# Kernel tuning notes

Hardware: AMD Instinct MI355X
Metric: run time of the kernel (lower is better)

The kernel has to match this reference:

```python
import jax, jax.numpy as jnp
import numpy as np

NUM_HEADS = 32
NUM_FEATURES = 512
CPH = NUM_FEATURES // NUM_HEADS  # 16


def _grouped_1x1(x_flat, w, b, groups):
    # x_flat: (B, Cin); w: (Cout, Cin//groups); b: (Cout,)
    B, Cin = x_flat.shape
    Cout = w.shape[0]
    xg = x_flat.reshape(B, groups, Cin // groups)
    wg = w.reshape(groups, Cout // groups, Cin // groups)
    out = jnp.einsum('bgi,goi->bgo', xg, wg).reshape(B, Cout) + b
    return out


def _attend(x, w, b):
    # x: (B, C, H, W, Z) zero-mean input; w: (num_heads, CPH); b: (num_heads,)
    B, C, H, W, Z = x.shape
    N = H * W * Z
    xr = x.reshape(B, NUM_HEADS, CPH, N)
    # grouped 1x1 conv producing one attention logit map per head
    logits = jnp.einsum('bhcn,hc->bhn', xr, w) + b[None, :, None]
    attn = jax.nn.softmax(logits, axis=-1)  # softmax over spatial
    res = jnp.einsum('bhcn,bhn->bhc', xr, attn)  # weighted pooling
    return res.reshape(B, C, 1, 1, 1)


def setup_inputs() -> dict:
    key = jax.random.key(0)
    ks = jax.random.split(key, 7)
    C = NUM_FEATURES
    x = jax.random.normal(ks[0], (4, C, 32, 32, 32), dtype=jnp.float32)
    # P module: conv1 C->C/2 groups=32, conv2 C/2->C groups=32 (kaiming-like scale)
    pw1 = jax.random.normal(ks[1], (C // 2, C // NUM_HEADS), dtype=jnp.float32) * np.float32(np.sqrt(2.0 / (C // 2)))
    pb1 = jnp.zeros((C // 2,), dtype=jnp.float32)
    pw2 = jax.random.normal(ks[2], (C, (C // 2) // NUM_HEADS), dtype=jnp.float32) * np.float32(np.sqrt(2.0 / C))
    pb2 = jnp.zeros((C,), dtype=jnp.float32)
    kw = jax.random.normal(ks[3], (NUM_HEADS, CPH), dtype=jnp.float32) * np.float32(np.sqrt(2.0 / NUM_HEADS))
    kb = jnp.zeros((NUM_HEADS,), dtype=jnp.float32)
    qw = jax.random.normal(ks[4], (NUM_HEADS, CPH), dtype=jnp.float32) * np.float32(np.sqrt(2.0 / NUM_HEADS))
    qb = jnp.zeros((NUM_HEADS,), dtype=jnp.float32)
    return {"x": x, "pw1": pw1, "pb1": pb1, "pw2": pw2, "pb2": pb2,
            "kw": kw, "kb": kb, "qw": qw, "qb": qb}


def reference(x, pw1, pb1, pw2, pb2, kw, kb, qw, qb):
    B, C, H, W, Z = x.shape
    mu = x.mean(axis=(2, 3, 4), keepdims=True)  # (B,C,1,1,1)
    x_mu = x - mu
    # P: grouped bottleneck MLP on mu with sigmoid gate
    h1 = jax.nn.relu(_grouped_1x1(mu.reshape(B, C), pw1, pb1, NUM_HEADS))
    P = jax.nn.sigmoid(_grouped_1x1(h1, pw2, pb2, NUM_HEADS)).reshape(B, C, 1, 1, 1)
    K = _attend(x_mu, kw, kb)
    Q = _attend(x_mu, qw, qb)
    y = (x + K - Q) * P
    dp = jnp.mean(K * Q, axis=1, keepdims=True)  # (B,1,1,1,1)
    return (y, dp)
```

## Files before the change

### kernel.cpp

```cpp
#include <hip/hip_runtime.h>
#include <math.h>

namespace {

constexpr int B = 4;
constexpr int C = 512;
constexpr int NH = 32;
constexpr int CPH = 16;
constexpr int N = 32 * 32 * 32;
constexpr int NPW = 128;
constexpr long YSIZE = (long)B * C * N;

typedef float f4v __attribute__((ext_vector_type(4)));

__device__ inline float wrs(float v) {
#pragma unroll
  for (int o = 32; o > 0; o >>= 1) v += __shfl_xor(v, o);
  return v;
}

template <int CTRL>
__device__ __forceinline__ float dppAdd(float v) {
  const int r = __builtin_amdgcn_update_dpp(
      0, __float_as_int(v), CTRL, 0xF, 0xF, true);
  return v + __int_as_float(r);
}
__device__ __forceinline__ float waveSum(float v) {
  v = dppAdd<0xB1>(v);
  v = dppAdd<0x4E>(v);
  v = dppAdd<0x124>(v);
  v = dppAdd<0x128>(v);
  v += __shfl_xor(v, 16);
  v += __shfl_xor(v, 32);
  return v;
}

__global__ __launch_bounds__(256, 4) void kA(const float* __restrict__ x,
                                             const float* __restrict__ kw,
                                             const float* __restrict__ qw,
                                             float* __restrict__ prec) {
  const int b = blockIdx.z, h = blockIdx.y, j = blockIdx.x;
  const int t = threadIdx.x, lane = t & 63, wid = t >> 6;
  const float* xs = x + ((long)(b * C + h * CPH)) * N + (long)j * 1024 + t * 4;

  float4 xv[CPH];
#pragma unroll
  for (int c = 0; c < CPH; ++c) xv[c] = *(const float4*)(xs + (long)c * N);

  float4 lk = make_float4(0.f, 0.f, 0.f, 0.f);
  float4 lq = make_float4(0.f, 0.f, 0.f, 0.f);
#pragma unroll
  for (int c = 0; c < CPH; ++c) {
    const float wkc = kw[h * CPH + c], wqc = qw[h * CPH + c];
    lk.x += xv[c].x * wkc; lk.y += xv[c].y * wkc;
    lk.z += xv[c].z * wkc; lk.w += xv[c].w * wkc;
    lq.x += xv[c].x * wqc; lq.y += xv[c].y * wqc;
    lq.z += xv[c].z * wqc; lq.w += xv[c].w * wqc;
  }
  const float4 ek = make_float4(__expf(lk.x), __expf(lk.y),
                                __expf(lk.z), __expf(lk.w));
  const float4 eq = make_float4(__expf(lq.x), __expf(lq.y),
                                __expf(lq.z), __expf(lq.w));
  float sK = waveSum((ek.x + ek.y) + (ek.z + ek.w));
  float sQ = waveSum((eq.x + eq.y) + (eq.z + eq.w));

  float outv = 0.f;
#pragma unroll
  for (int c = 0; c < CPH; ++c) {
    float dk = (xv[c].x * ek.x + xv[c].y * ek.y) + (xv[c].z * ek.z + xv[c].w * ek.w);
    float dq = (xv[c].x * eq.x + xv[c].y * eq.y) + (xv[c].z * eq.z + xv[c].w * eq.w);
    float cs = (xv[c].x + xv[c].y) + (xv[c].z + xv[c].w);
    dk = waveSum(dk);
    dq = waveSum(dq);
    cs = waveSum(cs);
    if (lane == c)      outv = dk;
    if (lane == c + 16) outv = dq;
    if (lane == c + 32) outv = cs;
  }
  if (lane == 48) outv = sK;
  if (lane == 49) outv = sQ;

  const long pj = ((long)(b * NH + h)) * NPW + j * 4 + wid;
  prec[pj * 64 + lane] = outv;
}

__global__ __launch_bounds__(512) void k4(const float* __restrict__ prec,
                                          const float* __restrict__ pw1,
                                          const float* __restrict__ pb1,
                                          const float* __restrict__ pw2,
                                          const float* __restrict__ pb2,
                                          float* __restrict__ scale,
                                          float* __restrict__ offset,
                                          float* __restrict__ dpOut) {
  const int b = blockIdx.x;
  const int c = threadIdx.x;
  const int h = c >> 4, i = c & 15;
  const float* rec = prec + ((long)(b * NH + h)) * NPW * 64;

  float dk = 0.f, dq = 0.f, cs = 0.f, sk = 0.f, sq = 0.f;
  for (int j = 0; j < NPW; ++j) {
    dk += rec[j * 64 + i];
    dq += rec[j * 64 + 16 + i];
    cs += rec[j * 64 + 32 + i];
    sk += rec[j * 64 + 48];
    sq += rec[j * 64 + 49];
  }
  const float mu = cs * (1.f / N);
  const float Kv = dk / sk - mu;
  const float Qv = dq / sq - mu;

  __shared__ float muS[C], h1S[256];
  muS[c] = mu;
  __syncthreads();
  if (c < 256) {
    const int g = c >> 3;
    float a = pb1[c];
#pragma unroll
    for (int k = 0; k < 16; ++k) a += muS[g * 16 + k] * pw1[c * 16 + k];
    h1S[c] = fmaxf(a, 0.f);
  }
  __syncthreads();
  float a = pb2[c];
  const int g2 = c >> 4;
#pragma unroll
  for (int k = 0; k < 8; ++k) a += h1S[g2 * 8 + k] * pw2[c * 8 + k];
  const float P = 1.f / (1.f + __expf(-a));
  scale[b * C + c] = P;
  offset[b * C + c] = (Kv - Qv) * P;

  float p = wrs(Kv * Qv);
  __shared__ float pS[8];
  const int lane = c & 63, wid = c >> 6;
  if (lane == 0) pS[wid] = p;
  __syncthreads();
  if (c == 0) {
    float tot = 0.f;
    for (int w = 0; w < 8; ++w) tot += pS[w];
    dpOut[b] = tot * (1.f / C);
  }
}

__global__ __launch_bounds__(256) void k5(const float* __restrict__ x,
                                          const float* __restrict__ scale,
                                          const float* __restrict__ offset,
                                          float* __restrict__ y) {
  const int b = blockIdx.z, cc = blockIdx.y;
  const int t = threadIdx.x;
  const long base = ((long)(b * C + cc)) * N + (long)blockIdx.x * 4096;
  const float s = scale[b * C + cc], o = offset[b * C + cc];
#pragma unroll
  for (int k = 0; k < 4; ++k) {
    const long i = base + (long)(k * 256 + t) * 4;
    const float4 v = *(const float4*)(x + i);
    f4v w;
    w.x = v.x * s + o; w.y = v.y * s + o;
    w.z = v.z * s + o; w.w = v.w * s + o;
    __builtin_nontemporal_store(w, (f4v*)(y + i));
  }
}

}

extern "C" void kernel_launch(void* const* d_in, const int* in_sizes, int n_in,
                              void* d_out, int out_size, void* d_ws, size_t ws_size,
                              hipStream_t stream) {
  const float* x   = (const float*)d_in[0];
  const float* pw1 = (const float*)d_in[1];
  const float* pb1 = (const float*)d_in[2];
  const float* pw2 = (const float*)d_in[3];
  const float* pb2 = (const float*)d_in[4];
  const float* kw  = (const float*)d_in[5];
  const float* qw  = (const float*)d_in[7];
  float* out = (float*)d_out;
  float* ws  = (float*)d_ws;

  float* scale  = ws;
  float* offset = ws + 2048;

  constexpr long PREC = (long)B * NH * NPW * 64;
  float* prec;
  if (ws_size >= (size_t)(4096 + PREC) * sizeof(float)) {
    prec = ws + 4096;
  } else {
    prec = out;
  }

  hipLaunchKernelGGL(kA, dim3(N / 1024, NH, B), dim3(256), 0, stream,
                     x, kw, qw, prec);
  hipLaunchKernelGGL(k4, dim3(B), dim3(C), 0, stream,
                     prec, pw1, pb1, pw2, pb2, scale, offset, out + YSIZE);
  hipLaunchKernelGGL(k5, dim3(N / 4096, C, B), dim3(256), 0, stream,
                     x, scale, offset, out);
}
```

Measured before the change: 150.3 us.

## Replace full-wave reductions with 16-lane row sums and reverse k5 block order

The attention-pooling kernel now reduces only within 16-lane DPP rows and no longer does the two cross-row shuffles. Each row writes its partial sums as float4 records, which quadruples the number of partial records. The reduce kernel reads these with float4 loads and gets the softmax denominators through shared memory. The elementwise output kernel walks its blocks in reverse so it first touches the tail of x, which is likely still in cache from the first kernel. In exchange, the partial-record buffer grows fourfold and the serial reduction loop gets longer.

```diff
diff --git a/kernel.cpp b/kernel.cpp
--- a/kernel.cpp
+++ b/kernel.cpp
@@ -8,7 +8,8 @@
 constexpr int NH = 32;
 constexpr int CPH = 16;
 constexpr int N = 32 * 32 * 32;
-constexpr int NPW = 128;
+constexpr int NJ = 32;
+constexpr int NREC = NJ * 4 * 4;
 constexpr long YSIZE = (long)B * C * N;
 
 typedef float f4v __attribute__((ext_vector_type(4)));
@@ -25,13 +26,11 @@
       0, __float_as_int(v), CTRL, 0xF, 0xF, true);
   return v + __int_as_float(r);
 }
-__device__ __forceinline__ float waveSum(float v) {
+__device__ __forceinline__ float rowSum16(float v) {
   v = dppAdd<0xB1>(v);
   v = dppAdd<0x4E>(v);
   v = dppAdd<0x124>(v);
   v = dppAdd<0x128>(v);
-  v += __shfl_xor(v, 16);
-  v += __shfl_xor(v, 32);
   return v;
 }
 
@@ -41,6 +40,7 @@
                                              float* __restrict__ prec) {
   const int b = blockIdx.z, h = blockIdx.y, j = blockIdx.x;
   const int t = threadIdx.x, lane = t & 63, wid = t >> 6;
+  const int p = lane & 15;
   const float* xs = x + ((long)(b * C + h * CPH)) * N + (long)j * 1024 + t * 4;
 
   float4 xv[CPH];
@@ -61,27 +61,26 @@
                                 __expf(lk.z), __expf(lk.w));
   const float4 eq = make_float4(__expf(lq.x), __expf(lq.y),
                                 __expf(lq.z), __expf(lq.w));
-  float sK = waveSum((ek.x + ek.y) + (ek.z + ek.w));
-  float sQ = waveSum((eq.x + eq.y) + (eq.z + eq.w));
+  const float sKr = rowSum16((ek.x + ek.y) + (ek.z + ek.w));
+  const float sQr = rowSum16((eq.x + eq.y) + (eq.z + eq.w));
 
-  float outv = 0.f;
+  float o0 = 0.f, o1 = 0.f, o2 = 0.f, o3 = 0.f;
 #pragma unroll
   for (int c = 0; c < CPH; ++c) {
     float dk = (xv[c].x * ek.x + xv[c].y * ek.y) + (xv[c].z * ek.z + xv[c].w * ek.w);
     float dq = (xv[c].x * eq.x + xv[c].y * eq.y) + (xv[c].z * eq.z + xv[c].w * eq.w);
     float cs = (xv[c].x + xv[c].y) + (xv[c].z + xv[c].w);
-    dk = waveSum(dk);
-    dq = waveSum(dq);
-    cs = waveSum(cs);
-    if (lane == c)      outv = dk;
-    if (lane == c + 16) outv = dq;
-    if (lane == c + 32) outv = cs;
+    dk = rowSum16(dk);
+    dq = rowSum16(dq);
+    cs = rowSum16(cs);
+    if (p == c) { o0 = dk; o1 = dq; o2 = cs; }
   }
-  if (lane == 48) outv = sK;
-  if (lane == 49) outv = sQ;
+  if (p == 0) o3 = sKr;
+  if (p == 1) o3 = sQr;
 
-  const long pj = ((long)(b * NH + h)) * NPW + j * 4 + wid;
-  prec[pj * 64 + lane] = outv;
+  const long ridx = ((((long)(b * NH + h)) * NJ + j) * 4 + wid) * 4 + (lane >> 4);
+  f4v r; r.x = o0; r.y = o1; r.z = o2; r.w = o3;
+  *(f4v*)(prec + ridx * 64 + p * 4) = r;
 }
 
 __global__ __launch_bounds__(512) void k4(const float* __restrict__ prec,
@@ -95,16 +94,19 @@
   const int b = blockIdx.x;
   const int c = threadIdx.x;
   const int h = c >> 4, i = c & 15;
-  const float* rec = prec + ((long)(b * NH + h)) * NPW * 64;
+  const float4* rec4 = (const float4*)prec + ((long)(b * NH + h)) * NREC * 16;
 
-  float dk = 0.f, dq = 0.f, cs = 0.f, sk = 0.f, sq = 0.f;
-  for (int j = 0; j < NPW; ++j) {
-    dk += rec[j * 64 + i];
-    dq += rec[j * 64 + 16 + i];
-    cs += rec[j * 64 + 32 + i];
-    sk += rec[j * 64 + 48];
-    sq += rec[j * 64 + 49];
+  float dk = 0.f, dq = 0.f, cs = 0.f, sacc = 0.f;
+  for (int j = 0; j < NREC; ++j) {
+    const float4 r = rec4[j * 16 + i];
+    dk += r.x; dq += r.y; cs += r.z; sacc += r.w;
   }
+  __shared__ float skS[NH], sqS[NH];
+  if (i == 0) skS[h] = sacc;
+  if (i == 1) sqS[h] = sacc;
+  __syncthreads();
+  const float sk = skS[h], sq = sqS[h];
+
   const float mu = cs * (1.f / N);
   const float Kv = dk / sk - mu;
   const float Qv = dq / sq - mu;
@@ -128,10 +130,10 @@
   scale[b * C + c] = P;
   offset[b * C + c] = (Kv - Qv) * P;
 
-  float p = wrs(Kv * Qv);
+  float pdp = wrs(Kv * Qv);
   __shared__ float pS[8];
   const int lane = c & 63, wid = c >> 6;
-  if (lane == 0) pS[wid] = p;
+  if (lane == 0) pS[wid] = pdp;
   __syncthreads();
   if (c == 0) {
     float tot = 0.f;
@@ -144,9 +146,11 @@
                                           const float* __restrict__ scale,
                                           const float* __restrict__ offset,
                                           float* __restrict__ y) {
-  const int b = blockIdx.z, cc = blockIdx.y;
+  const int b = B - 1 - (int)blockIdx.z;
+  const int cc = C - 1 - (int)blockIdx.y;
+  const int jr = (N / 4096 - 1) - (int)blockIdx.x;
   const int t = threadIdx.x;
-  const long base = ((long)(b * C + cc)) * N + (long)blockIdx.x * 4096;
+  const long base = ((long)(b * C + cc)) * N + (long)jr * 4096;
   const float s = scale[b * C + cc], o = offset[b * C + cc];
 #pragma unroll
   for (int k = 0; k < 4; ++k) {
@@ -177,7 +181,7 @@
   float* scale  = ws;
   float* offset = ws + 2048;
 
-  constexpr long PREC = (long)B * NH * NPW * 64;
+  constexpr long PREC = (long)B * NH * NREC * 64;
   float* prec;
   if (ws_size >= (size_t)(4096 + PREC) * sizeof(float)) {
     prec = ws + 4096;
@@ -185,7 +189,7 @@
     prec = out;
   }
 
-  hipLaunchKernelGGL(kA, dim3(N / 1024, NH, B), dim3(256), 0, stream,
+  hipLaunchKernelGGL(kA, dim3(NJ, NH, B), dim3(256), 0, stream,
                      x, kw, qw, prec);
   hipLaunchKernelGGL(k4, dim3(B), dim3(C), 0, stream,
                      prec, pw1, pb1, pw2, pb2, scale, offset, out + YSIZE);
```

After: 178.0 us. +18.5%, slower.
